# Performance work log

Measured on AMD Instinct MI355X. Metric: run time of the kernel, lower is better.

The kernel has to match this reference:

```python
import jax, jax.numpy as jnp
import numpy as np

N = 100000      # num graph nodes
E = 1600000     # num edges (avg degree 16)
IN = 128        # in_channels
H = 128         # hidden_channels
B = 4096        # query batch
CTX = 20        # context set length (indices[:, 3:])


def setup_inputs() -> dict:
    key = jax.random.key(0)
    ks = jax.random.split(key, 16)
    inp = {
        "indices": jax.random.randint(ks[0], (B, 3 + CTX), 0, N, dtype=jnp.int64),
        "src": jax.random.randint(ks[1], (E,), 0, N, dtype=jnp.int32),
        "dst": jax.random.randint(ks[2], (E,), 0, N, dtype=jnp.int32),
        "w": jax.random.uniform(ks[3], (E,), dtype=jnp.float32),
        # learned params
        "ndata": jax.random.normal(ks[4], (N, IN), dtype=jnp.float32),
        "W1": jax.random.normal(ks[5], (H, IN), dtype=jnp.float32) * (1.0 / np.sqrt(IN)),
        "b1": jnp.zeros((H,), jnp.float32),
        "W2": jax.random.normal(ks[6], (H, H), dtype=jnp.float32) * (1.0 / np.sqrt(H)),
        "b2": jnp.zeros((H,), jnp.float32),
        "eps": jnp.zeros((2,), jnp.float32),  # learn_eps, one per GINConv
        "Wc1": jax.random.normal(ks[7], (H, 3 * H), dtype=jnp.float32) * (1.0 / np.sqrt(3 * H)),
        "bc1": jnp.zeros((H,), jnp.float32),
        "Wc2": jax.random.normal(ks[8], (H // 2, H), dtype=jnp.float32) * (1.0 / np.sqrt(H)),
        "bc2": jnp.zeros((H // 2,), jnp.float32),
        "Wc3": jax.random.normal(ks[9], (1, H // 2), dtype=jnp.float32) * (1.0 / np.sqrt(H // 2)),
        "bc3": jnp.zeros((1,), jnp.float32),
    }
    return inp


def _gin_conv(x, src, dst, w, deg, eps, W, b):
    # DGL GINConv(mean, learn_eps): h = lin((1+eps)*x + mean_{in-edges}(w_e * x_src))
    msg = w[:, None] * x[src]                                   # [E, D]
    agg = jax.ops.segment_sum(msg, dst, num_segments=N) / deg   # [N, D]
    return ((1.0 + eps) * x + agg) @ W.T + b


def reference(indices, src, dst, w, ndata, W1, b1, W2, b2, eps,
              Wc1, bc1, Wc2, bc2, Wc3, bc3):
    deg = jax.ops.segment_sum(jnp.ones((E,), ndata.dtype), dst, num_segments=N)
    deg = jnp.maximum(deg, 1.0)[:, None]

    x = ndata
    x = jax.nn.relu(_gin_conv(x, src, dst, w, deg, eps[0], W1, b1))  # dropout inactive (eval)
    x = _gin_conv(x, src, dst, w, deg, eps[1], W2, b2)               # last layer: no relu
    x = x.at[0].set(0.0)                                             # x[0] = zeros

    ing1 = x[indices[:, 0]]   # [B, H]
    ing2 = x[indices[:, 1]]   # [B, H]

    # embed_context: mean over nonzero-index context members
    ctx_idx = indices[:, 3:]                                   # [B, CTX]
    ctx_sum = x[ctx_idx].sum(axis=1)                           # [B, H]
    norm = jnp.maximum((ctx_idx > 0).sum(axis=1), 1).astype(x.dtype)[:, None]
    ctx = ctx_sum / norm

    y = jnp.concatenate([ing1, ing2, ctx], axis=1)             # [B, 3H]
    y = jax.nn.relu(y @ Wc1.T + bc1)
    y = jax.nn.relu(y @ Wc2.T + bc2)
    y = y @ Wc3.T + bc3                                        # [B, 1]
    return y
```

## Files before the change

kernel.cpp:

```cpp
#include <hip/hip_runtime.h>
#include <hip/hip_fp16.h>


#define CONV_NPB 32
#define FIN_EPB 8

struct __align__(8)  h4 { __half2 a, b; };
struct __align__(16) h8 { __half2 a, b, c, d; };

__device__ __forceinline__ float4 h4f(h4 u) {
  return make_float4(__low2float(u.a), __high2float(u.a),
                     __low2float(u.b), __high2float(u.b));
}
__device__ __forceinline__ h4 f4h(float4 v) {
  h4 u; u.a = __floats2half2_rn(v.x, v.y); u.b = __floats2half2_rn(v.z, v.w);
  return u;
}

__global__ void inithist_kernel(const float* __restrict__ W1, const float* __restrict__ W2,
                                const float* __restrict__ Wc1, const float* __restrict__ Wc2,
                                const float* __restrict__ ndata, __half* __restrict__ xh0,
                                float* __restrict__ Wt1, float* __restrict__ Wt2,
                                float* __restrict__ Wc1t, float* __restrict__ Wc2t,
                                const int* __restrict__ dst, int* __restrict__ cnt,
                                int* __restrict__ rank, int n, int E) {
  int i = blockIdx.x * blockDim.x + threadIdx.x;
  int e = i * 4;
  if (e + 3 < E) {
    const int4 d = *(const int4*)&dst[e];
    int4 r;
    r.x = atomicAdd(&cnt[d.x], 1);
    r.y = atomicAdd(&cnt[d.y], 1);
    r.z = atomicAdd(&cnt[d.z], 1);
    r.w = atomicAdd(&cnt[d.w], 1);
    *(int4*)&rank[e] = r;
  } else {
    for (; e < E; ++e) rank[e] = atomicAdd(&cnt[dst[e]], 1);
  }
  const int cbase = i * 8;
  if (cbase < n * 128) {
    const float4 v0 = *(const float4*)&ndata[cbase];
    const float4 v1 = *(const float4*)&ndata[cbase + 4];
    h8 u;
    u.a = __floats2half2_rn(v0.x, v0.y);
    u.b = __floats2half2_rn(v0.z, v0.w);
    u.c = __floats2half2_rn(v1.x, v1.y);
    u.d = __floats2half2_rn(v1.z, v1.w);
    *(h8*)&xh0[cbase] = u;
  }
  if (i < 16384) {
    int f = i >> 7, k = i & 127;
    Wt1[k * 128 + f] = W1[i];
  } else if (i < 32768) {
    int j = i - 16384; int f = j >> 7, k = j & 127;
    Wt2[k * 128 + f] = W2[j];
  } else if (i < 81920) {
    int j = i - 32768; int f = j / 384, k = j % 384;
    Wc1t[k * 128 + f] = Wc1[j];
  } else if (i < 90112) {
    int j = i - 81920; int f = j >> 7, k = j & 127;
    Wc2t[k * 64 + f] = Wc2[j];
  }
}

__global__ void scan1_kernel(const int* __restrict__ cnt, int* __restrict__ prow,
                             int* __restrict__ bsum, int n) {
  __shared__ int smem[256];
  const int t = threadIdx.x;
  const int base = blockIdx.x * 2048 + t * 8;
  int v[8];
  int s = 0;
#pragma unroll
  for (int j = 0; j < 8; ++j) {
    int idx = base + j;
    v[j] = (idx < n) ? ((cnt[idx] + 7) & ~7) : 0;
    s += v[j];
  }
  smem[t] = s;
  __syncthreads();
  for (int off = 1; off < 256; off <<= 1) {
    int add = (t >= off) ? smem[t - off] : 0;
    __syncthreads();
    smem[t] += add;
    __syncthreads();
  }
  int run = smem[t] - s;
  if (t == 255) bsum[blockIdx.x] = smem[255];
#pragma unroll
  for (int j = 0; j < 8; ++j) {
    int idx = base + j;
    if (idx < n) prow[idx] = run;
    run += v[j];
  }
}

__global__ void scan2_kernel(int* __restrict__ bsum, int nb) {
  const int t = threadIdx.x;
  if (nb <= 64) {
    const int orig = (t < nb) ? bsum[t] : 0;
    int v = orig;
#pragma unroll
    for (int off = 1; off < 64; off <<= 1) {
      int u = __shfl_up(v, off);
      if (t >= off) v += u;
    }
    if (t == nb - 1) bsum[nb] = v;
    if (t < nb) bsum[t] = v - orig;
  } else if (t == 0) {
    int run = 0;
    for (int i = 0; i < nb; ++i) { int v = bsum[i]; bsum[i] = run; run += v; }
    bsum[nb] = run;
  }
}

__global__ void scatter_kernel(const int* __restrict__ src, const int* __restrict__ dst,
                               const float* __restrict__ w, const int* __restrict__ prow,
                               const int* __restrict__ bsum, const int* __restrict__ rank,
                               const int* __restrict__ cnt,
                               int2* __restrict__ epack, int E, int n) {
  const int i = blockIdx.x * blockDim.x + threadIdx.x;
  int e = i * 4;
  if (e + 3 < E) {
    const int4 d = *(const int4*)&dst[e];
    const int4 s = *(const int4*)&src[e];
    const float4 wv = *(const float4*)&w[e];
    const int4 r = *(const int4*)&rank[e];
    epack[prow[d.x] + bsum[d.x >> 11] + r.x] = make_int2(s.x, __float_as_int(wv.x));
    epack[prow[d.y] + bsum[d.y >> 11] + r.y] = make_int2(s.y, __float_as_int(wv.y));
    epack[prow[d.z] + bsum[d.z >> 11] + r.z] = make_int2(s.z, __float_as_int(wv.z));
    epack[prow[d.w] + bsum[d.w >> 11] + r.w] = make_int2(s.w, __float_as_int(wv.w));
  } else {
    for (; e < E; ++e) {
      const int d = dst[e];
      epack[prow[d] + bsum[d >> 11] + rank[e]] = make_int2(src[e], __float_as_int(w[e]));
    }
  }
  if (i < n) {
    const int c = cnt[i];
    const int start = prow[i] + bsum[i >> 11] + c;
    const int pc = ((c + 7) & ~7) - c;
    for (int j = 0; j < pc; ++j) epack[start + j] = make_int2(0, 0);
  }
}

__launch_bounds__(256, 8)
__global__ void conv_kernel(const float* __restrict__ xinf, const __half* __restrict__ xinh,
                            __half* __restrict__ xouth,
                            const int* __restrict__ prow, const int* __restrict__ bsum,
                            const int* __restrict__ cnt,
                            const int2* __restrict__ epack,
                            const float* __restrict__ Wt,
                            const float* __restrict__ bias, const float* __restrict__ eps,
                            int epsidx, int dorelu, int zerorow0, int selff32,
                            int n, int nchunk) {
  __shared__ float xm[CONV_NPB * 128];
  __shared__ int rp_s[CONV_NPB + 1];
  const int t = threadIdx.x;
  const int nb = blockIdx.x * CONV_NPB;
  const float epsv = 1.0f + eps[epsidx];

#pragma unroll
  for (int i = 0; i < 4; ++i)
    *(float4*)&xm[(t + i * 256) * 4] = make_float4(0.f, 0.f, 0.f, 0.f);
  if (t <= CONV_NPB) {
    const int node = nb + t;
    rp_s[t] = (node >= n) ? bsum[nchunk] : (prow[node] + bsum[node >> 11]);
  }
  __syncthreads();

  {
    const int L = t >> 5;
    const int lane = t & 31;
    const int f0 = lane * 4;
    const int e0 = rp_s[0], eT = rp_s[CONV_NPB];
    const int nbat = (eT - e0) >> 3;
    const int chunk = (((nbat + 7) >> 3)) << 3;
    const int jb = e0 + L * chunk;
    const int je = min(jb + chunk, eT);
    if (jb < je) {
      const int4* ep4 = (const int4*)epack;
      int r = 0;
      while (rp_s[r + 1] <= jb) ++r;
      float4 acc = make_float4(0.f, 0.f, 0.f, 0.f);
      int h = jb >> 1;
      int4 q0 = ep4[h + 0];
      int4 q1 = ep4[h + 1];
      int4 q2 = ep4[h + 2];
      int4 q3 = ep4[h + 3];
      for (int j = jb; j < je; j += 8) {
        if (rp_s[r + 1] <= j) {
          float* bp = &xm[r * 128 + lane];
          atomicAdd(bp + 0,  acc.x);
          atomicAdd(bp + 32, acc.y);
          atomicAdd(bp + 64, acc.z);
          atomicAdd(bp + 96, acc.w);
          acc = make_float4(0.f, 0.f, 0.f, 0.f);
          do { ++r; } while (rp_s[r + 1] <= j);
        }
        const h4 u0 = *(const h4*)&xinh[(size_t)q0.x * 128 + f0];
        const h4 u1 = *(const h4*)&xinh[(size_t)q0.z * 128 + f0];
        const h4 u2 = *(const h4*)&xinh[(size_t)q1.x * 128 + f0];
        const h4 u3 = *(const h4*)&xinh[(size_t)q1.z * 128 + f0];
        const h4 u4 = *(const h4*)&xinh[(size_t)q2.x * 128 + f0];
        const h4 u5 = *(const h4*)&xinh[(size_t)q2.z * 128 + f0];
        const h4 u6 = *(const h4*)&xinh[(size_t)q3.x * 128 + f0];
        const h4 u7 = *(const h4*)&xinh[(size_t)q3.z * 128 + f0];
        const float w0 = __int_as_float(q0.y), w1 = __int_as_float(q0.w);
        const float w2 = __int_as_float(q1.y), w3 = __int_as_float(q1.w);
        const float w4 = __int_as_float(q2.y), w5 = __int_as_float(q2.w);
        const float w6 = __int_as_float(q3.y), w7 = __int_as_float(q3.w);
        const int jn = (j + 8 < je) ? (j + 8) : j;
        const int hn = jn >> 1;
        q0 = ep4[hn + 0];
        q1 = ep4[hn + 1];
        q2 = ep4[hn + 2];
        q3 = ep4[hn + 3];
        const float4 a0 = h4f(u0), a1 = h4f(u1), a2 = h4f(u2), a3 = h4f(u3);
        const float4 a4 = h4f(u4), a5 = h4f(u5), a6 = h4f(u6), a7 = h4f(u7);
        acc.x += w0 * a0.x + w1 * a1.x + w2 * a2.x + w3 * a3.x
               + w4 * a4.x + w5 * a5.x + w6 * a6.x + w7 * a7.x;
        acc.y += w0 * a0.y + w1 * a1.y + w2 * a2.y + w3 * a3.y
               + w4 * a4.y + w5 * a5.y + w6 * a6.y + w7 * a7.y;
        acc.z += w0 * a0.z + w1 * a1.z + w2 * a2.z + w3 * a3.z
               + w4 * a4.z + w5 * a5.z + w6 * a6.z + w7 * a7.z;
        acc.w += w0 * a0.w + w1 * a1.w + w2 * a2.w + w3 * a3.w
               + w4 * a4.w + w5 * a5.w + w6 * a6.w + w7 * a7.w;
      }
      float* bp = &xm[r * 128 + lane];
      atomicAdd(bp + 0,  acc.x);
      atomicAdd(bp + 32, acc.y);
      atomicAdd(bp + 64, acc.z);
      atomicAdd(bp + 96, acc.w);
    }
  }
  __syncthreads();

  {
    float4 m[4];
#pragma unroll
    for (int q = 0; q < 4; ++q) {
      const int task = t + q * 256;
      const int r = task >> 5;
      const int fg = task & 31;
      m[q].x = xm[r * 128 + fg];
      m[q].y = xm[r * 128 + 32 + fg];
      m[q].z = xm[r * 128 + 64 + fg];
      m[q].w = xm[r * 128 + 96 + fg];
    }
    __syncthreads();
#pragma unroll
    for (int q = 0; q < 4; ++q) {
      const int task = t + q * 256;
      const int r = task >> 5;
      const int fg = task & 31;
      const int f0 = fg * 4;
      const int node = nb + r;
      float4 v = make_float4(0.f, 0.f, 0.f, 0.f);
      if (node < n) {
        const int d = cnt[node];
        const float rdeg = 1.0f / (float)(d > 1 ? d : 1);
        float4 xv;
        if (selff32) xv = *(const float4*)&xinf[(size_t)node * 128 + f0];
        else         xv = h4f(*(const h4*)&xinh[(size_t)node * 128 + f0]);
        v.x = epsv * xv.x + m[q].x * rdeg;
        v.y = epsv * xv.y + m[q].y * rdeg;
        v.z = epsv * xv.z + m[q].z * rdeg;
        v.w = epsv * xv.w + m[q].w * rdeg;
      }
      *(float4*)&xm[r * 128 + f0] = v;
    }
  }
  __syncthreads();

  {
    const int fg = t & 31;
    const int rg = t >> 5;
    const int f0 = fg * 4;
    const int r0 = rg * 4;
    float4 acc[4];
#pragma unroll
    for (int r = 0; r < 4; ++r) acc[r] = make_float4(0.f, 0.f, 0.f, 0.f);
    for (int k = 0; k < 128; k += 4) {
      const float4 w0 = *(const float4*)&Wt[(k + 0) * 128 + f0];
      const float4 w1 = *(const float4*)&Wt[(k + 1) * 128 + f0];
      const float4 w2 = *(const float4*)&Wt[(k + 2) * 128 + f0];
      const float4 w3 = *(const float4*)&Wt[(k + 3) * 128 + f0];
#pragma unroll
      for (int r = 0; r < 4; ++r) {
        const float4 xv = *(const float4*)&xm[(r0 + r) * 128 + k];
        acc[r].x += xv.x * w0.x + xv.y * w1.x + xv.z * w2.x + xv.w * w3.x;
        acc[r].y += xv.x * w0.y + xv.y * w1.y + xv.z * w2.y + xv.w * w3.y;
        acc[r].z += xv.x * w0.z + xv.y * w1.z + xv.z * w2.z + xv.w * w3.z;
        acc[r].w += xv.x * w0.w + xv.y * w1.w + xv.z * w2.w + xv.w * w3.w;
      }
    }
    const float4 bv = *(const float4*)&bias[f0];
#pragma unroll
    for (int r = 0; r < 4; ++r) {
      const int node = nb + r0 + r;
      if (node < n) {
        float4 v;
        v.x = acc[r].x + bv.x;
        v.y = acc[r].y + bv.y;
        v.z = acc[r].z + bv.z;
        v.w = acc[r].w + bv.w;
        if (dorelu) {
          v.x = fmaxf(v.x, 0.f); v.y = fmaxf(v.y, 0.f);
          v.z = fmaxf(v.z, 0.f); v.w = fmaxf(v.w, 0.f);
        }
        if (zerorow0 && node == 0) { v.x = 0.f; v.y = 0.f; v.z = 0.f; v.w = 0.f; }
        *(h4*)&xouth[(size_t)node * 128 + f0] = f4h(v);
      }
    }
  }
}

__launch_bounds__(256, 4)
__global__ void final_kernel(const __half* __restrict__ x2h, const int* __restrict__ indices,
                             const float* __restrict__ Wc1t, const float* __restrict__ bc1,
                             const float* __restrict__ Wc2t, const float* __restrict__ bc2,
                             const float* __restrict__ Wc3, const float* __restrict__ bc3,
                             float* __restrict__ out) {
  __shared__ float ysm[FIN_EPB * 384];
  __shared__ float h1s[FIN_EPB * 128];
  __shared__ float h2s[FIN_EPB * 64];
  __shared__ int ind_s[FIN_EPB * 23];
  __shared__ float ccs[FIN_EPB];
  const int t = threadIdx.x;
  const int b0 = blockIdx.x * FIN_EPB;

  if (t < FIN_EPB * 23) ind_s[t] = indices[(size_t)b0 * 23 + t];
  __syncthreads();
  if (t < FIN_EPB) {
    int cc = 0;
#pragma unroll
    for (int j = 0; j < 20; ++j) cc += (ind_s[t * 23 + 3 + j] > 0) ? 1 : 0;
    ccs[t] = 1.0f / (float)(cc > 0 ? cc : 1);
  }
  __syncthreads();

  {
#pragma unroll
    for (int q = 0; q < 2; ++q) {
      const int s = t + q * 256;
      const int e = s >> 6;
      const int hf = (s >> 5) & 1;
      const int fg = s & 31;
      const int idx = ind_s[e * 23 + hf];
      const h4 u = *(const h4*)&x2h[(size_t)idx * 128 + fg * 4];
      *(float4*)&ysm[e * 384 + hf * 128 + fg * 4] = h4f(u);
    }
    const int e = t >> 5;
    const int fg = t & 31;
    float4 acc = make_float4(0.f, 0.f, 0.f, 0.f);
#pragma unroll
    for (int j = 0; j < 20; ++j) {
      const int cj = ind_s[e * 23 + 3 + j];
      const h4 u = *(const h4*)&x2h[(size_t)cj * 128 + fg * 4];
      const float4 a = h4f(u);
      acc.x += a.x; acc.y += a.y; acc.z += a.z; acc.w += a.w;
    }
    const float sc = ccs[e];
    acc.x *= sc; acc.y *= sc; acc.z *= sc; acc.w *= sc;
    *(float4*)&ysm[e * 384 + 256 + fg * 4] = acc;
  }
  __syncthreads();

  {
    const int f1 = t & 127;
    const int eh = t >> 7;
    float acc[4];
    const float b = bc1[f1];
#pragma unroll
    for (int i = 0; i < 4; ++i) acc[i] = b;
    for (int k = 0; k < 384; k += 4) {
      const float wv0 = Wc1t[(k + 0) * 128 + f1];
      const float wv1 = Wc1t[(k + 1) * 128 + f1];
      const float wv2 = Wc1t[(k + 2) * 128 + f1];
      const float wv3 = Wc1t[(k + 3) * 128 + f1];
#pragma unroll
      for (int i = 0; i < 4; ++i) {
        const float4 yv = *(const float4*)&ysm[(eh * 4 + i) * 384 + k];
        acc[i] += yv.x * wv0 + yv.y * wv1 + yv.z * wv2 + yv.w * wv3;
      }
    }
#pragma unroll
    for (int i = 0; i < 4; ++i)
      h1s[(eh * 4 + i) * 128 + f1] = fmaxf(acc[i], 0.f);
  }
  __syncthreads();

  {
    const int f2 = t & 63;
    const int eg = t >> 6;
    float acc[2];
    const float b = bc2[f2];
#pragma unroll
    for (int i = 0; i < 2; ++i) acc[i] = b;
    for (int k = 0; k < 128; k += 4) {
      const float wv0 = Wc2t[(k + 0) * 64 + f2];
      const float wv1 = Wc2t[(k + 1) * 64 + f2];
      const float wv2 = Wc2t[(k + 2) * 64 + f2];
      const float wv3 = Wc2t[(k + 3) * 64 + f2];
#pragma unroll
      for (int i = 0; i < 2; ++i) {
        const float4 hv = *(const float4*)&h1s[(eg * 2 + i) * 128 + k];
        acc[i] += hv.x * wv0 + hv.y * wv1 + hv.z * wv2 + hv.w * wv3;
      }
    }
#pragma unroll
    for (int i = 0; i < 2; ++i)
      h2s[(eg * 2 + i) * 64 + f2] = fmaxf(acc[i], 0.f);
  }
  __syncthreads();

  {
    const int e = t >> 5;
    const int l = t & 31;
    float p = h2s[e * 64 + l] * Wc3[l] + h2s[e * 64 + l + 32] * Wc3[l + 32];
#pragma unroll
    for (int o = 16; o > 0; o >>= 1) p += __shfl_down(p, o, 32);
    if (l == 0) out[b0 + e] = p + bc3[0];
  }
}

extern "C" void kernel_launch(void* const* d_in, const int* in_sizes, int n_in,
                              void* d_out, int out_size, void* d_ws, size_t ws_size,
                              hipStream_t stream) {
  const int* indices = (const int*)d_in[0];
  const int* src = (const int*)d_in[1];
  const int* dst = (const int*)d_in[2];
  const float* w = (const float*)d_in[3];
  const float* ndata = (const float*)d_in[4];
  const float* W1 = (const float*)d_in[5];
  const float* b1 = (const float*)d_in[6];
  const float* W2 = (const float*)d_in[7];
  const float* b2 = (const float*)d_in[8];
  const float* eps = (const float*)d_in[9];
  const float* Wc1 = (const float*)d_in[10];
  const float* bc1 = (const float*)d_in[11];
  const float* Wc2 = (const float*)d_in[12];
  const float* bc2 = (const float*)d_in[13];
  const float* Wc3 = (const float*)d_in[14];
  const float* bc3 = (const float*)d_in[15];
  float* out = (float*)d_out;

  const int E = in_sizes[1];
  const int N = in_sizes[4] / 128;
  const int B = in_sizes[0] / 23;

  char* ws = (char*)d_ws;
  size_t off = 0;
  auto alloc = [&](size_t bytes) -> char* {
    char* p = ws + off;
    off = (off + bytes + 255) & ~(size_t)255;
    return p;
  };
  const size_t Epad = (size_t)E + 8 * (size_t)N;
  int* cnt = (int*)alloc((size_t)N * 4);
  int* prow = (int*)alloc((size_t)(N + 1) * 4);
  int* rank = (int*)alloc((size_t)E * 4);
  int* bsum = (int*)alloc(256 * 4);
  int2* epack = (int2*)alloc(Epad * 8);
  __half* xh0 = (__half*)alloc((size_t)N * 128 * 2);
  __half* x1h = (__half*)alloc((size_t)N * 128 * 2);
  float* Wt1 = (float*)alloc(16384 * 4);
  float* Wt2 = (float*)alloc(16384 * 4);
  float* Wc1t = (float*)alloc(49152 * 4);
  float* Wc2t = (float*)alloc(8192 * 4);
  __half* x2h = xh0;

  hipMemsetAsync(cnt, 0, (size_t)N * 4, stream);

  const int ncast = (N * 128 + 7) / 8;
  const int Eq = (E + 3) / 4;
  int ninit = (N > 90112) ? N : 90112;
  if (ncast > ninit) ninit = ncast;
  if (Eq > ninit) ninit = Eq;
  inithist_kernel<<<(ninit + 255) / 256, 256, 0, stream>>>(
      W1, W2, Wc1, Wc2, ndata, xh0, Wt1, Wt2, Wc1t, Wc2t, dst, cnt, rank, N, E);

  const int nchunk = (N + 2047) / 2048;
  scan1_kernel<<<nchunk, 256, 0, stream>>>(cnt, prow, bsum, N);
  scan2_kernel<<<1, 64, 0, stream>>>(bsum, nchunk);
  const int nsc = (Eq > N) ? Eq : N;
  scatter_kernel<<<(nsc + 255) / 256, 256, 0, stream>>>(src, dst, w, prow, bsum, rank, cnt, epack, E, N);

  const int nconv = (N + CONV_NPB - 1) / CONV_NPB;
  conv_kernel<<<nconv, 256, 0, stream>>>(ndata, xh0, x1h, prow, bsum, cnt, epack,
                                         Wt1, b1, eps, 0, 1, 0, 1, N, nchunk);
  conv_kernel<<<nconv, 256, 0, stream>>>(nullptr, x1h, x2h, prow, bsum, cnt, epack,
                                         Wt2, b2, eps, 1, 0, 1, 0, N, nchunk);

  final_kernel<<<B / FIN_EPB, 256, 0, stream>>>(x2h, indices, Wc1t, bc1, Wc2t, bc2, Wc3, bc3, out);
}
```

Measured before the change: 511.8 us.

## Restructure conv gather: wave64 per-lane half2 layout, LDS-staged edges, double-buffered gathers

Reworks the edge aggregation in conv_kernel. Each block first stages up to 1024 packed edges into shared memory. Work is then split over 4 wave64s instead of 8 groups of 32 lanes, and each lane gathers one half2 per neighbor, so a wave reads a full 256-byte row. Gathers are double-buffered, with the next batch of 8 neighbors issued before the current one is consumed, to hide latency. The accumulator layout becomes interleaved, which removes the register-shuffle re-read phase and one sync. The costs are more shared memory and registers, and occupancy bounds lowered to 6 blocks.

```diff
diff --git a/kernel.cpp b/kernel.cpp
--- a/kernel.cpp
+++ b/kernel.cpp
@@ -143,7 +143,7 @@
   }
 }
 
-__launch_bounds__(256, 8)
+__launch_bounds__(256, 6)
 __global__ void conv_kernel(const float* __restrict__ xinf, const __half* __restrict__ xinh,
                             __half* __restrict__ xouth,
                             const int* __restrict__ prow, const int* __restrict__ bsum,
@@ -154,6 +154,7 @@
                             int epsidx, int dorelu, int zerorow0, int selff32,
                             int n, int nchunk) {
   __shared__ float xm[CONV_NPB * 128];
+  __shared__ int4 dscb[512];
   __shared__ int rp_s[CONV_NPB + 1];
   const int t = threadIdx.x;
   const int nb = blockIdx.x * CONV_NPB;
@@ -168,86 +169,105 @@
   }
   __syncthreads();
 
-  {
-    const int L = t >> 5;
-    const int lane = t & 31;
-    const int f0 = lane * 4;
-    const int e0 = rp_s[0], eT = rp_s[CONV_NPB];
-    const int nbat = (eT - e0) >> 3;
-    const int chunk = (((nbat + 7) >> 3)) << 3;
-    const int jb = e0 + L * chunk;
-    const int je = min(jb + chunk, eT);
-    if (jb < je) {
+  const int e0 = rp_s[0], eT = rp_s[CONV_NPB];
+  {
+    const int tot = eT - e0;
+    const int staged = (tot < 1024) ? tot : 1024;
+    const int2* ep2 = (const int2*)epack;
+    int2* d2 = (int2*)dscb;
+    for (int o = t; o < staged; o += 256) d2[o] = ep2[e0 + o];
+  }
+  __syncthreads();
+
+  {
+    const int wid = t >> 6;
+    const int lane = t & 63;
+    const int nsb = (eT - e0) >> 3;
+    const int sbLDS = ((eT - e0) < 1024 ? (eT - e0) : 1024) >> 3;
+    const int csb = (nsb + 3) >> 2;
+    const int sb0 = wid * csb;
+    const int sbend = min(sb0 + csb, nsb);
+    if (sb0 < sbend) {
       const int4* ep4 = (const int4*)epack;
+      const int h0 = e0 >> 1;
+      const unsigned int* xu = (const unsigned int*)xinh;
       int r = 0;
-      while (rp_s[r + 1] <= jb) ++r;
-      float4 acc = make_float4(0.f, 0.f, 0.f, 0.f);
-      int h = jb >> 1;
-      int4 q0 = ep4[h + 0];
-      int4 q1 = ep4[h + 1];
-      int4 q2 = ep4[h + 2];
-      int4 q3 = ep4[h + 3];
-      for (int j = jb; j < je; j += 8) {
-        if (rp_s[r + 1] <= j) {
-          float* bp = &xm[r * 128 + lane];
-          atomicAdd(bp + 0,  acc.x);
-          atomicAdd(bp + 32, acc.y);
-          atomicAdd(bp + 64, acc.z);
-          atomicAdd(bp + 96, acc.w);
-          acc = make_float4(0.f, 0.f, 0.f, 0.f);
-          do { ++r; } while (rp_s[r + 1] <= j);
+      { const int j0 = e0 + sb0 * 8; while (rp_s[r + 1] <= j0) ++r; }
+      float ax = 0.f, ay = 0.f;
+
+#define LOADD(sb_, q0, q1, q2, q3) do {                                   \
+      if ((sb_) < sbLDS) {                                                \
+        q0 = dscb[(sb_) * 4 + 0]; q1 = dscb[(sb_) * 4 + 1];               \
+        q2 = dscb[(sb_) * 4 + 2]; q3 = dscb[(sb_) * 4 + 3];               \
+      } else {                                                            \
+        q0 = ep4[h0 + (sb_) * 4 + 0]; q1 = ep4[h0 + (sb_) * 4 + 1];       \
+        q2 = ep4[h0 + (sb_) * 4 + 2]; q3 = ep4[h0 + (sb_) * 4 + 3];       \
+      } } while (0)
+
+#define GATHER8(q0, q1, q2, q3, uu, wt) do {                              \
+      wt[0] = __int_as_float(q0.y); wt[1] = __int_as_float(q0.w);         \
+      wt[2] = __int_as_float(q1.y); wt[3] = __int_as_float(q1.w);         \
+      wt[4] = __int_as_float(q2.y); wt[5] = __int_as_float(q2.w);         \
+      wt[6] = __int_as_float(q3.y); wt[7] = __int_as_float(q3.w);         \
+      uu[0] = xu[(size_t)q0.x * 64 + lane];                               \
+      uu[1] = xu[(size_t)q0.z * 64 + lane];                               \
+      uu[2] = xu[(size_t)q1.x * 64 + lane];                               \
+      uu[3] = xu[(size_t)q1.z * 64 + lane];                               \
+      uu[4] = xu[(size_t)q2.x * 64 + lane];                               \
+      uu[5] = xu[(size_t)q2.z * 64 + lane];                               \
+      uu[6] = xu[(size_t)q3.x * 64 + lane];                               \
+      uu[7] = xu[(size_t)q3.z * 64 + lane];                               \
+    } while (0)
+
+#define CONSUME8(uu, wt) do {                                             \
+      _Pragma("unroll")                                                   \
+      for (int k = 0; k < 8; ++k) {                                       \
+        const float2 f = __half22float2(*(const __half2*)&uu[k]);         \
+        ax += wt[k] * f.x; ay += wt[k] * f.y;                             \
+      } } while (0)
+
+#define ROWWALK(sb_) do {                                                 \
+      const int j = e0 + (sb_) * 8;                                       \
+      if (rp_s[r + 1] <= j) {                                             \
+        atomicAdd(&xm[r * 128 + lane * 2],     ax);                       \
+        atomicAdd(&xm[r * 128 + lane * 2 + 1], ay);                       \
+        ax = 0.f; ay = 0.f;                                               \
+        do { ++r; } while (rp_s[r + 1] <= j);                             \
+      } } while (0)
+
+      int4 qa0, qa1, qa2, qa3, qb0, qb1, qb2, qb3;
+      unsigned int uA[8], uB[8];
+      float wA[8], wB[8];
+      LOADD(sb0, qa0, qa1, qa2, qa3);
+      GATHER8(qa0, qa1, qa2, qa3, uA, wA);
+      int sb = sb0;
+      while (true) {
+        if (sb + 1 < sbend) {
+          LOADD(sb + 1, qb0, qb1, qb2, qb3);
+          GATHER8(qb0, qb1, qb2, qb3, uB, wB);
         }
-        const h4 u0 = *(const h4*)&xinh[(size_t)q0.x * 128 + f0];
-        const h4 u1 = *(const h4*)&xinh[(size_t)q0.z * 128 + f0];
-        const h4 u2 = *(const h4*)&xinh[(size_t)q1.x * 128 + f0];
-        const h4 u3 = *(const h4*)&xinh[(size_t)q1.z * 128 + f0];
-        const h4 u4 = *(const h4*)&xinh[(size_t)q2.x * 128 + f0];
-        const h4 u5 = *(const h4*)&xinh[(size_t)q2.z * 128 + f0];
-        const h4 u6 = *(const h4*)&xinh[(size_t)q3.x * 128 + f0];
-        const h4 u7 = *(const h4*)&xinh[(size_t)q3.z * 128 + f0];
-        const float w0 = __int_as_float(q0.y), w1 = __int_as_float(q0.w);
-        const float w2 = __int_as_float(q1.y), w3 = __int_as_float(q1.w);
-        const float w4 = __int_as_float(q2.y), w5 = __int_as_float(q2.w);
-        const float w6 = __int_as_float(q3.y), w7 = __int_as_float(q3.w);
-        const int jn = (j + 8 < je) ? (j + 8) : j;
-        const int hn = jn >> 1;
-        q0 = ep4[hn + 0];
-        q1 = ep4[hn + 1];
-        q2 = ep4[hn + 2];
-        q3 = ep4[hn + 3];
-        const float4 a0 = h4f(u0), a1 = h4f(u1), a2 = h4f(u2), a3 = h4f(u3);
-        const float4 a4 = h4f(u4), a5 = h4f(u5), a6 = h4f(u6), a7 = h4f(u7);
-        acc.x += w0 * a0.x + w1 * a1.x + w2 * a2.x + w3 * a3.x
-               + w4 * a4.x + w5 * a5.x + w6 * a6.x + w7 * a7.x;
-        acc.y += w0 * a0.y + w1 * a1.y + w2 * a2.y + w3 * a3.y
-               + w4 * a4.y + w5 * a5.y + w6 * a6.y + w7 * a7.y;
-        acc.z += w0 * a0.z + w1 * a1.z + w2 * a2.z + w3 * a3.z
-               + w4 * a4.z + w5 * a5.z + w6 * a6.z + w7 * a7.z;
-        acc.w += w0 * a0.w + w1 * a1.w + w2 * a2.w + w3 * a3.w
-               + w4 * a4.w + w5 * a5.w + w6 * a6.w + w7 * a7.w;
+        ROWWALK(sb);
+        CONSUME8(uA, wA);
+        ++sb; if (sb >= sbend) break;
+        if (sb + 1 < sbend) {
+          LOADD(sb + 1, qa0, qa1, qa2, qa3);
+          GATHER8(qa0, qa1, qa2, qa3, uA, wA);
+        }
+        ROWWALK(sb);
+        CONSUME8(uB, wB);
+        ++sb; if (sb >= sbend) break;
       }
-      float* bp = &xm[r * 128 + lane];
-      atomicAdd(bp + 0,  acc.x);
-      atomicAdd(bp + 32, acc.y);
-      atomicAdd(bp + 64, acc.z);
-      atomicAdd(bp + 96, acc.w);
-    }
-  }
-  __syncthreads();
-
-  {
-    float4 m[4];
-#pragma unroll
-    for (int q = 0; q < 4; ++q) {
-      const int task = t + q * 256;
-      const int r = task >> 5;
-      const int fg = task & 31;
-      m[q].x = xm[r * 128 + fg];
-      m[q].y = xm[r * 128 + 32 + fg];
-      m[q].z = xm[r * 128 + 64 + fg];
-      m[q].w = xm[r * 128 + 96 + fg];
-    }
-    __syncthreads();
+      atomicAdd(&xm[r * 128 + lane * 2],     ax);
+      atomicAdd(&xm[r * 128 + lane * 2 + 1], ay);
+#undef LOADD
+#undef GATHER8
+#undef CONSUME8
+#undef ROWWALK
+    }
+  }
+  __syncthreads();
+
+  {
 #pragma unroll
     for (int q = 0; q < 4; ++q) {
       const int task = t + q * 256;
@@ -262,10 +282,11 @@
         float4 xv;
         if (selff32) xv = *(const float4*)&xinf[(size_t)node * 128 + f0];
         else         xv = h4f(*(const h4*)&xinh[(size_t)node * 128 + f0]);
-        v.x = epsv * xv.x + m[q].x * rdeg;
-        v.y = epsv * xv.y + m[q].y * rdeg;
-        v.z = epsv * xv.z + m[q].z * rdeg;
-        v.w = epsv * xv.w + m[q].w * rdeg;
+        const float4 m = *(const float4*)&xm[r * 128 + f0];
+        v.x = epsv * xv.x + m.x * rdeg;
+        v.y = epsv * xv.y + m.y * rdeg;
+        v.z = epsv * xv.z + m.z * rdeg;
+        v.w = epsv * xv.w + m.w * rdeg;
       }
       *(float4*)&xm[r * 128 + f0] = v;
     }
@@ -470,7 +491,7 @@
   float* Wc2t = (float*)alloc(8192 * 4);
   __half* x2h = xh0;
 
-  hipMemsetAsync(cnt, 0, (size_t)N * 4, stream);
+  (void)hipMemsetAsync(cnt, 0, (size_t)N * 4, stream);
 
   const int ncast = (N * 128 + 7) / 8;
   const int Eq = (E + 3) / 4;
```

After: 528.8 us. +3.3%, slower.
